# Kernel tuning notes

Hardware: AMD Instinct MI355X
Metric: run time of the kernel (lower is better)

## Reference

```python
import jax, jax.numpy as jnp
import numpy as np

B = 262144
N = 256      # mode size of every TT core
R = 8        # tt_rank
D = 8        # number of cores = 7 state dims + 1 action dim
STD = 0.001


def setup_inputs() -> dict:
    key = jax.random.key(0)
    ks = jax.random.split(key, D + 2)
    inp = {}
    # TT cores: G0 (1,N,R), G1..G6 (R,N,R), G7 (R,N,1)
    inp["G0"] = jax.random.normal(ks[0], (1, N, R), dtype=jnp.float32) * STD
    for k in range(1, D - 1):
        inp[f"G{k}"] = jax.random.normal(ks[k], (R, N, R), dtype=jnp.float32) * STD
    inp[f"G{D-1}"] = jax.random.normal(ks[D - 1], (R, N, 1), dtype=jnp.float32) * STD
    inp["states"] = jax.random.randint(ks[D], (B, 7), 0, N, dtype=jnp.int32)
    inp["actions"] = jax.random.randint(ks[D + 1], (B,), 0, N, dtype=jnp.int32)
    return inp


def reference(G0, G1, G2, G3, G4, G5, G6, G7, states, actions):
    # mode 'q_sa': concat state indices with action index -> (B, D)
    idx = jnp.concatenate(
        [states.reshape(-1, 7), actions.reshape(-1, 1)], axis=1
    )
    cores = [G0, G1, G2, G3, G4, G5, G6, G7]
    # t3f.gather_nd: chain of per-core gathers + tiny batched matmuls.
    # vec starts as the gathered slice of the first core: (B, R)
    vec = cores[0][0, idx[:, 0], :]
    for k in range(1, D):
        # gather slices along mode axis: (B, r_prev, r_next)
        sl = jnp.transpose(jnp.take(cores[k], idx[:, k], axis=1), (1, 0, 2))
        vec = jnp.einsum("br,brs->bs", vec, sl)
    # final vec has shape (B, 1); Q(s,a) values per batch element
    return vec[:, 0]
```

## Files before the change

kernel.cpp:

```cpp
#include <hip/hip_runtime.h>


#define NN 256
#define RR 8
#define NR 2048
#define U67_OFF 524288
#define GT_OFF  1048576
#define GT_CORE 16384

__device__ __forceinline__ unsigned short f2bf_rne(float f) {
    unsigned int u = __float_as_uint(f);
    u += 0x7FFFu + ((u >> 16) & 1u);
    return (unsigned short)(u >> 16);
}

__device__ __forceinline__ uint4 pack8bf(const float* a) {
    return make_uint4(
        f2bf_rne(a[0]) | ((unsigned int)f2bf_rne(a[1]) << 16),
        f2bf_rne(a[2]) | ((unsigned int)f2bf_rne(a[3]) << 16),
        f2bf_rne(a[4]) | ((unsigned int)f2bf_rne(a[5]) << 16),
        f2bf_rne(a[6]) | ((unsigned int)f2bf_rne(a[7]) << 16));
}

__global__ __launch_bounds__(256) void build_tables(
    const float* __restrict__ G0, const float* __restrict__ G1,
    const float* __restrict__ G2, const float* __restrict__ G3,
    const float* __restrict__ G4, const float* __restrict__ G5,
    const float* __restrict__ G6, const float* __restrict__ G7,
    unsigned short* __restrict__ wsb) {
    const int t = threadIdx.x;
    const int bid = blockIdx.x;

    if (bid < NN) {
        const int n0 = bid, n1 = t;
        float acc[RR] = {0.f,0.f,0.f,0.f,0.f,0.f,0.f,0.f};
#pragma unroll
        for (int r = 0; r < RR; ++r) {
            float ar = G0[n0 * RR + r];
            const float4* p = (const float4*)(G1 + r * NR + n1 * RR);
            float4 x = p[0], y = p[1];
            acc[0] += ar * x.x; acc[1] += ar * x.y;
            acc[2] += ar * x.z; acc[3] += ar * x.w;
            acc[4] += ar * y.x; acc[5] += ar * y.y;
            acc[6] += ar * y.z; acc[7] += ar * y.w;
        }
        *(uint4*)(wsb + n0 * 2048 + n1 * 8) = pack8bf(acc);
    } else if (bid < 2 * NN) {
        const int n6 = bid - NN, n7 = t;
        float g7v[RR];
#pragma unroll
        for (int s = 0; s < RR; ++s) g7v[s] = G7[s * NN + n7];
        float u[RR];
#pragma unroll
        for (int r = 0; r < RR; ++r) {
            float acc = 0.f;
#pragma unroll
            for (int s = 0; s < RR; ++s)
                acc += G6[r * NR + n6 * RR + s] * g7v[s];
            u[r] = acc;
        }
        *(uint4*)(wsb + U67_OFF + n6 * 2048 + n7 * 8) = pack8bf(u);
    } else {
        const int q = bid - 2 * NN;
        const int k = q >> 3;
        const int chunk = q & 7;
        const float* __restrict__ Gk =
            (k == 0) ? G2 : (k == 1) ? G3 : (k == 2) ? G4 : G5;
        const int n = chunk * 32 + (t >> 3);
        const int r = t & 7;
        const float4* src = (const float4*)(Gk + r * NR + n * RR);
        float4 x = src[0], y = src[1];
        float a[8] = {x.x, x.y, x.z, x.w, y.x, y.y, y.z, y.w};
        *(uint4*)(wsb + GT_OFF + k * GT_CORE + r * 2048 + n * 8) = pack8bf(a);
    }
}

#define BF2F_LO(u) __uint_as_float((u) << 16)
#define BF2F_HI(u) __uint_as_float((u) & 0xFFFF0000u)

#define LP(q0, q1, k, nk, rp)                                               \
    do {                                                                    \
        const uint4* _p = l4 + (k) * 2048 + (nk) + (rp) * 512;              \
        q0 = _p[0];                                                         \
        q1 = _p[256];                                                       \
    } while (0)

#define FP(q0, q1, rp)                                                      \
    do {                                                                    \
        const float wa = v[2 * (rp)], wb = v[2 * (rp) + 1];                 \
        acc[0] += wa * BF2F_LO(q0.x); acc[0] += wb * BF2F_LO(q1.x);         \
        acc[1] += wa * BF2F_HI(q0.x); acc[1] += wb * BF2F_HI(q1.x);         \
        acc[2] += wa * BF2F_LO(q0.y); acc[2] += wb * BF2F_LO(q1.y);         \
        acc[3] += wa * BF2F_HI(q0.y); acc[3] += wb * BF2F_HI(q1.y);         \
        acc[4] += wa * BF2F_LO(q0.z); acc[4] += wb * BF2F_LO(q1.z);         \
        acc[5] += wa * BF2F_HI(q0.z); acc[5] += wb * BF2F_HI(q1.z);         \
        acc[6] += wa * BF2F_LO(q0.w); acc[6] += wb * BF2F_LO(q1.w);         \
        acc[7] += wa * BF2F_HI(q0.w); acc[7] += wb * BF2F_HI(q1.w);         \
    } while (0)

#define ENDST                                                               \
    do {                                                                    \
        _Pragma("unroll") for (int i = 0; i < 8; ++i) {                     \
            v[i] = acc[i]; acc[i] = 0.f;                                    \
        }                                                                   \
    } while (0)

#define CHAIN_FULL(uvx, uex, c2, c3, c4, c5, bx, actx)                      \
    do {                                                                    \
        float v[8], acc[8];                                                 \
        v[0] = BF2F_LO(uvx.x); v[1] = BF2F_HI(uvx.x);                       \
        v[2] = BF2F_LO(uvx.y); v[3] = BF2F_HI(uvx.y);                       \
        v[4] = BF2F_LO(uvx.z); v[5] = BF2F_HI(uvx.z);                       \
        v[6] = BF2F_LO(uvx.w); v[7] = BF2F_HI(uvx.w);                       \
        _Pragma("unroll") for (int i = 0; i < 8; ++i) acc[i] = 0.f;         \
        uint4 X0, X1, Y0, Y1, Z0, Z1;                                       \
        LP(X0, X1, 0, c2, 0);                                               \
        LP(Y0, Y1, 0, c2, 1);                                               \
        LP(Z0, Z1, 0, c2, 2);  FP(X0, X1, 0);                               \
        LP(X0, X1, 0, c2, 3);  FP(Y0, Y1, 1);                               \
        LP(Y0, Y1, 1, c3, 0);  FP(Z0, Z1, 2);                               \
        LP(Z0, Z1, 1, c3, 1);  FP(X0, X1, 3);  ENDST;                       \
        LP(X0, X1, 1, c3, 2);  FP(Y0, Y1, 0);                               \
        LP(Y0, Y1, 1, c3, 3);  FP(Z0, Z1, 1);                               \
        LP(Z0, Z1, 2, c4, 0);  FP(X0, X1, 2);                               \
        LP(X0, X1, 2, c4, 1);  FP(Y0, Y1, 3);  ENDST;                       \
        LP(Y0, Y1, 2, c4, 2);  FP(Z0, Z1, 0);                               \
        LP(Z0, Z1, 2, c4, 3);  FP(X0, X1, 1);                               \
        LP(X0, X1, 3, c5, 0);  FP(Y0, Y1, 2);                               \
        LP(Y0, Y1, 3, c5, 1);  FP(Z0, Z1, 3);  ENDST;                       \
        LP(Z0, Z1, 3, c5, 2);  FP(X0, X1, 0);                               \
        LP(X0, X1, 3, c5, 3);  FP(Y0, Y1, 1);                               \
                               FP(Z0, Z1, 2);                               \
                               FP(X0, X1, 3);  ENDST;                       \
        float q = v[0] * BF2F_LO(uex.x) + v[1] * BF2F_HI(uex.x)             \
                + v[2] * BF2F_LO(uex.y) + v[3] * BF2F_HI(uex.y)             \
                + v[4] * BF2F_LO(uex.z) + v[5] * BF2F_HI(uex.z)             \
                + v[6] * BF2F_LO(uex.w) + v[7] * BF2F_HI(uex.w);            \
        if (actx) out[bx] = q;                                              \
    } while (0)

__global__ __launch_bounds__(512, 2) void tt_gather(
    const unsigned short* __restrict__ wsb,
    const int* __restrict__ states, const int* __restrict__ actions,
    float* __restrict__ out, int B) {
    __shared__ unsigned short lut[4 * GT_CORE];

    const int t = threadIdx.x;
    const int bA = blockIdx.x * 1024 + t;
    const int bB = bA + 512;
    const bool actA = (bA < B), actB = (bB < B);
    const int baseA = actA ? bA * 7 : 0;
    const int baseB = actB ? bB * 7 : 0;

    const int a0 = states[baseA + 0] & 255, e0 = states[baseB + 0] & 255;
    const int a1 = states[baseA + 1] & 255, e1 = states[baseB + 1] & 255;
    const int a2 = states[baseA + 2] & 255, e2 = states[baseB + 2] & 255;
    const int a3 = states[baseA + 3] & 255, e3 = states[baseB + 3] & 255;
    const int a4 = states[baseA + 4] & 255, e4 = states[baseB + 4] & 255;
    const int a5 = states[baseA + 5] & 255, e5 = states[baseB + 5] & 255;
    const int a6 = states[baseA + 6] & 255, e6 = states[baseB + 6] & 255;
    const int aa = actions[actA ? bA : 0] & 255;
    const int ea = actions[actB ? bB : 0] & 255;

    const uint4 uvA = *(const uint4*)(wsb + a0 * 2048 + a1 * 8);
    const uint4 ueA = *(const uint4*)(wsb + U67_OFF + a6 * 2048 + aa * 8);
    const uint4 uvB = *(const uint4*)(wsb + e0 * 2048 + e1 * 8);
    const uint4 ueB = *(const uint4*)(wsb + U67_OFF + e6 * 2048 + ea * 8);

    {
        const uint4* src = (const uint4*)(wsb + GT_OFF);
        uint4* dst = (uint4*)lut;
#pragma unroll
        for (int i = 0; i < 16; ++i) dst[t + (i << 9)] = src[t + (i << 9)];
    }
    __syncthreads();

    const uint4* l4 = (const uint4*)lut;

    CHAIN_FULL(uvA, ueA, a2, a3, a4, a5, bA, actA);
    CHAIN_FULL(uvB, ueB, e2, e3, e4, e5, bB, actB);
}

extern "C" void kernel_launch(void* const* d_in, const int* in_sizes, int n_in,
                              void* d_out, int out_size, void* d_ws, size_t ws_size,
                              hipStream_t stream) {
    const float* G0 = (const float*)d_in[0];
    const float* G1 = (const float*)d_in[1];
    const float* G2 = (const float*)d_in[2];
    const float* G3 = (const float*)d_in[3];
    const float* G4 = (const float*)d_in[4];
    const float* G5 = (const float*)d_in[5];
    const float* G6 = (const float*)d_in[6];
    const float* G7 = (const float*)d_in[7];
    const int* states  = (const int*)d_in[8];
    const int* actions = (const int*)d_in[9];
    float* out = (float*)d_out;
    int B = in_sizes[9];

    unsigned short* wsb = (unsigned short*)d_ws;

    hipLaunchKernelGGL(build_tables, dim3(2 * NN + 32), dim3(256), 0, stream,
                       G0, G1, G2, G3, G4, G5, G6, G7, wsb);

    hipLaunchKernelGGL(tt_gather, dim3((B + 1023) / 1024), dim3(512), 0, stream,
                       wsb, states, actions, out, B);
}
```

Measured before the change: 90.36 us.

## Fuse table build and gather into one cooperative kernel with grid sync

Merges the table-building kernel into the gather kernel, launched cooperatively. Each block now converts cores G2..G5 to bf16 straight into shared memory instead of copying a prebuilt global table. The G0·G1 and G6·G7 pair tables are built by a grid-stride loop, followed by a grid-wide sync before the gathers. The intent is to drop the second kernel launch and the global round trip for the core tables. In exchange it adds a grid barrier and has every block redo the G2..G5 staging, and it needs all 256 blocks to be co-resident.

```diff
diff --git a/kernel.cpp b/kernel.cpp
--- a/kernel.cpp
+++ b/kernel.cpp
@@ -1,11 +1,13 @@
 #include <hip/hip_runtime.h>
-
+#include <hip/hip_cooperative_groups.h>
+
+
+namespace cg = cooperative_groups;
 
 #define NN 256
 #define RR 8
 #define NR 2048
 #define U67_OFF 524288
-#define GT_OFF  1048576
 #define GT_CORE 16384
 
 __device__ __forceinline__ unsigned short f2bf_rne(float f) {
@@ -22,61 +24,20 @@
         f2bf_rne(a[6]) | ((unsigned int)f2bf_rne(a[7]) << 16));
 }
 
-__global__ __launch_bounds__(256) void build_tables(
-    const float* __restrict__ G0, const float* __restrict__ G1,
-    const float* __restrict__ G2, const float* __restrict__ G3,
-    const float* __restrict__ G4, const float* __restrict__ G5,
-    const float* __restrict__ G6, const float* __restrict__ G7,
-    unsigned short* __restrict__ wsb) {
-    const int t = threadIdx.x;
-    const int bid = blockIdx.x;
-
-    if (bid < NN) {
-        const int n0 = bid, n1 = t;
-        float acc[RR] = {0.f,0.f,0.f,0.f,0.f,0.f,0.f,0.f};
-#pragma unroll
-        for (int r = 0; r < RR; ++r) {
-            float ar = G0[n0 * RR + r];
-            const float4* p = (const float4*)(G1 + r * NR + n1 * RR);
-            float4 x = p[0], y = p[1];
-            acc[0] += ar * x.x; acc[1] += ar * x.y;
-            acc[2] += ar * x.z; acc[3] += ar * x.w;
-            acc[4] += ar * y.x; acc[5] += ar * y.y;
-            acc[6] += ar * y.z; acc[7] += ar * y.w;
-        }
-        *(uint4*)(wsb + n0 * 2048 + n1 * 8) = pack8bf(acc);
-    } else if (bid < 2 * NN) {
-        const int n6 = bid - NN, n7 = t;
-        float g7v[RR];
-#pragma unroll
-        for (int s = 0; s < RR; ++s) g7v[s] = G7[s * NN + n7];
-        float u[RR];
-#pragma unroll
-        for (int r = 0; r < RR; ++r) {
-            float acc = 0.f;
-#pragma unroll
-            for (int s = 0; s < RR; ++s)
-                acc += G6[r * NR + n6 * RR + s] * g7v[s];
-            u[r] = acc;
-        }
-        *(uint4*)(wsb + U67_OFF + n6 * 2048 + n7 * 8) = pack8bf(u);
-    } else {
-        const int q = bid - 2 * NN;
-        const int k = q >> 3;
-        const int chunk = q & 7;
-        const float* __restrict__ Gk =
-            (k == 0) ? G2 : (k == 1) ? G3 : (k == 2) ? G4 : G5;
-        const int n = chunk * 32 + (t >> 3);
-        const int r = t & 7;
-        const float4* src = (const float4*)(Gk + r * NR + n * RR);
-        float4 x = src[0], y = src[1];
-        float a[8] = {x.x, x.y, x.z, x.w, y.x, y.y, y.z, y.w};
-        *(uint4*)(wsb + GT_OFF + k * GT_CORE + r * 2048 + n * 8) = pack8bf(a);
-    }
-}
-
 #define BF2F_LO(u) __uint_as_float((u) << 16)
 #define BF2F_HI(u) __uint_as_float((u) & 0xFFFF0000u)
+
+#define STAGE_CORE(k, Gk)                                                   \
+    do {                                                                    \
+        _Pragma("unroll") for (int i = 0; i < 4; ++i) {                     \
+            const int p = (i << 9) + t;                        \
+            const int r = p >> 8, n = p & 255;                              \
+            const float4* sp = (const float4*)((Gk) + r * NR + n * RR);     \
+            float4 x = sp[0], y = sp[1];                                    \
+            float a8[8] = {x.x, x.y, x.z, x.w, y.x, y.y, y.z, y.w};         \
+            ((uint4*)lut)[(k) * 2048 + r * 256 + n] = pack8bf(a8);          \
+        }                                                                   \
+    } while (0)
 
 #define LP(q0, q1, k, nk, rp)                                               \
     do {                                                                    \
@@ -139,19 +100,29 @@
         if (actx) out[bx] = q;                                              \
     } while (0)
 
-__global__ __launch_bounds__(512, 2) void tt_gather(
-    const unsigned short* __restrict__ wsb,
+__global__ __launch_bounds__(512, 2) void tt_fused(
+    const float* __restrict__ G0, const float* __restrict__ G1,
+    const float* __restrict__ G6, const float* __restrict__ G7,
+    const float* __restrict__ G2, const float* __restrict__ G3,
+    const float* __restrict__ G4, const float* __restrict__ G5,
     const int* __restrict__ states, const int* __restrict__ actions,
-    float* __restrict__ out, int B) {
+    unsigned short* __restrict__ wsb, float* __restrict__ out, int B) {
     __shared__ unsigned short lut[4 * GT_CORE];
 
     const int t = threadIdx.x;
+    const int gtid = blockIdx.x * 512 + t;
+    const int gstride = gridDim.x * 512;
+
+    STAGE_CORE(0, G2);
+    STAGE_CORE(1, G3);
+    STAGE_CORE(2, G4);
+    STAGE_CORE(3, G5);
+
     const int bA = blockIdx.x * 1024 + t;
     const int bB = bA + 512;
     const bool actA = (bA < B), actB = (bB < B);
     const int baseA = actA ? bA * 7 : 0;
     const int baseB = actB ? bB * 7 : 0;
-
     const int a0 = states[baseA + 0] & 255, e0 = states[baseB + 0] & 255;
     const int a1 = states[baseA + 1] & 255, e1 = states[baseB + 1] & 255;
     const int a2 = states[baseA + 2] & 255, e2 = states[baseB + 2] & 255;
@@ -162,21 +133,50 @@
     const int aa = actions[actA ? bA : 0] & 255;
     const int ea = actions[actB ? bB : 0] & 255;
 
+    for (int u = gtid; u < 2 * NN * NN; u += gstride) {
+        if (u < NN * NN) {
+            const int n0 = u >> 8, n1 = u & 255;
+            float acc[RR] = {0.f,0.f,0.f,0.f,0.f,0.f,0.f,0.f};
+#pragma unroll
+            for (int r = 0; r < RR; ++r) {
+                float ar = G0[n0 * RR + r];
+                const float4* p = (const float4*)(G1 + r * NR + n1 * RR);
+                float4 x = p[0], y = p[1];
+                acc[0] += ar * x.x; acc[1] += ar * x.y;
+                acc[2] += ar * x.z; acc[3] += ar * x.w;
+                acc[4] += ar * y.x; acc[5] += ar * y.y;
+                acc[6] += ar * y.z; acc[7] += ar * y.w;
+            }
+            *(uint4*)(wsb + n0 * 2048 + n1 * 8) = pack8bf(acc);
+        } else {
+            const int w = u - NN * NN;
+            const int n6 = w >> 8, n7 = w & 255;
+            float g7v[RR];
+#pragma unroll
+            for (int s = 0; s < RR; ++s) g7v[s] = G7[s * NN + n7];
+            float uo[RR];
+#pragma unroll
+            for (int r = 0; r < RR; ++r) {
+                float acc = 0.f;
+#pragma unroll
+                for (int s = 0; s < RR; ++s)
+                    acc += G6[r * NR + n6 * RR + s] * g7v[s];
+                uo[r] = acc;
+            }
+            *(uint4*)(wsb + U67_OFF + n6 * 2048 + n7 * 8) = pack8bf(uo);
+        }
+    }
+
+    __threadfence();
+    cg::this_grid().sync();
+    __syncthreads();
+
     const uint4 uvA = *(const uint4*)(wsb + a0 * 2048 + a1 * 8);
     const uint4 ueA = *(const uint4*)(wsb + U67_OFF + a6 * 2048 + aa * 8);
     const uint4 uvB = *(const uint4*)(wsb + e0 * 2048 + e1 * 8);
     const uint4 ueB = *(const uint4*)(wsb + U67_OFF + e6 * 2048 + ea * 8);
 
-    {
-        const uint4* src = (const uint4*)(wsb + GT_OFF);
-        uint4* dst = (uint4*)lut;
-#pragma unroll
-        for (int i = 0; i < 16; ++i) dst[t + (i << 9)] = src[t + (i << 9)];
-    }
-    __syncthreads();
-
     const uint4* l4 = (const uint4*)lut;
-
     CHAIN_FULL(uvA, ueA, a2, a3, a4, a5, bA, actA);
     CHAIN_FULL(uvB, ueB, e2, e3, e4, e5, bB, actB);
 }
@@ -199,9 +199,11 @@
 
     unsigned short* wsb = (unsigned short*)d_ws;
 
-    hipLaunchKernelGGL(build_tables, dim3(2 * NN + 32), dim3(256), 0, stream,
-                       G0, G1, G2, G3, G4, G5, G6, G7, wsb);
-
-    hipLaunchKernelGGL(tt_gather, dim3((B + 1023) / 1024), dim3(512), 0, stream,
-                       wsb, states, actions, out, B);
-}
+    int nblk = (B + 1023) / 1024;
+    void* args[] = {
+        (void*)&G0, (void*)&G1, (void*)&G6, (void*)&G7,
+        (void*)&G2, (void*)&G3, (void*)&G4, (void*)&G5,
+        (void*)&states, (void*)&actions, (void*)&wsb, (void*)&out, (void*)&B};
+    hipLaunchCooperativeKernel((const void*)tt_fused, dim3(nblk), dim3(512),
+                               args, 0, stream);
+}
```

Measured after the change: 198.2 us. +119.4%, slower.
